# Kernel optimization log

Hardware: AMD Instinct MI355X
Metric: run time of the kernel (lower is better)

The kernel has to match this reference:

```python
import jax, jax.numpy as jnp
import numpy as np

B, N, DIM, POS, H = 8, 2048, 256, 128, 8
QK = DIM + POS  # 384
HD = DIM // H   # 32
SCALE = HD ** -0.5


def setup_inputs() -> dict:
    key = jax.random.key(0)
    ks = jax.random.split(key, 12)
    def lin(k, fan_in, fan_out):
        bound = 1.0 / np.sqrt(fan_in)
        kw, kb = jax.random.split(k)
        W = jax.random.uniform(kw, (fan_in, fan_out), jnp.float32, -bound, bound)
        b = jax.random.uniform(kb, (fan_out,), jnp.float32, -bound, bound)
        return W, b
    Wq, bq = lin(ks[0], QK, DIM)
    Wk, bk = lin(ks[1], QK, DIM)
    Wv, bv = lin(ks[2], DIM, DIM)
    Wp, bp = lin(ks[3], DIM, DIM)
    return {
        "x": jax.random.normal(ks[4], (B, N, DIM), jnp.float32),
        "pos_embed": jax.random.normal(ks[5], (B, N, POS), jnp.float32),
        "ln_g": jnp.ones((DIM,), jnp.float32),
        "ln_b": jnp.zeros((DIM,), jnp.float32),
        "Wq": Wq, "bq": bq,
        "Wk": Wk, "bk": bk,
        "Wv": Wv, "bv": bv,
        "Wp": Wp, "bp": bp,
    }


def _layernorm(x, g, b, eps=1e-5):
    mu = jnp.mean(x, axis=-1, keepdims=True)
    var = jnp.mean(jnp.square(x - mu), axis=-1, keepdims=True)
    return (x - mu) * jax.lax.rsqrt(var + eps) * g + b


def reference(x, pos_embed, ln_g, ln_b, Wq, bq, Wk, bk, Wv, bv, Wp, bp):
    short_cut = x
    xn = _layernorm(x, ln_g, ln_b)                       # [B,N,C]
    qk_in = jnp.concatenate([xn, pos_embed], axis=-1)    # [B,N,C+C']
    q = qk_in @ Wq + bq                                  # [B,N,C]
    k = qk_in @ Wk + bk
    v = xn @ Wv + bv
    def heads(t):
        return t.reshape(B, N, H, HD).transpose(0, 2, 1, 3)  # [B,H,N,d]
    q, k, v = heads(q), heads(k), heads(v)
    # scores cast to fp32 before scale+softmax, as in the original
    scores = jnp.einsum('bhid,bhjd->bhij', q, k).astype(jnp.float32) * SCALE
    attn = jax.nn.softmax(scores, axis=-1).astype(q.dtype)  # [B,H,N,N]
    out = jnp.einsum('bhij,bhjd->bhid', attn, v)             # [B,H,N,d]
    out = out.transpose(0, 2, 1, 3).reshape(B, N, DIM)       # [B,N,C]
    return short_cut + (out @ Wp + bp)
```

## Files before the change

kernel.cpp:

```cpp
#include <hip/hip_runtime.h>
#include <stdint.h>

#define DEVFN __device__ __forceinline__

typedef float f32x4 __attribute__((ext_vector_type(4)));
typedef float f32x2 __attribute__((ext_vector_type(2)));
typedef float f32x16 __attribute__((ext_vector_type(16)));
typedef short s16x8 __attribute__((ext_vector_type(8)));
typedef short s16x4 __attribute__((ext_vector_type(4)));
typedef unsigned int u32x4 __attribute__((ext_vector_type(4)));

using u32_g = __attribute__((address_space(1))) unsigned int;
using u32_l = __attribute__((address_space(3))) unsigned int;

DEVFN unsigned short f2bf(float f) {
  unsigned int u = __builtin_bit_cast(unsigned int, f);
  u += 0x7FFFu + ((u >> 16) & 1u);
  return (unsigned short)(u >> 16);
}

DEVFN f32x4 mfma16(s16x8 a, s16x8 b, f32x4 c) {
  return __builtin_amdgcn_mfma_f32_16x16x32_bf16(a, b, c, 0, 0, 0);
}

DEVFN f32x16 mfma32(s16x8 a, s16x8 b, f32x16 c) {
  return __builtin_amdgcn_mfma_f32_32x32x16_bf16(a, b, c, 0, 0, 0);
}

DEVFN void gl_lds16(const unsigned short* g, unsigned short* l) {
  __builtin_amdgcn_global_load_lds((const u32_g*)(uintptr_t)g,
                                   (u32_l*)(uintptr_t)l, 16, 0, 0);
}

#define QSCALE 0.25504370446096164f

__global__ void prep_kernel(const float* __restrict__ Wq, const float* __restrict__ bq,
                            const float* __restrict__ Wk, const float* __restrict__ bk,
                            const float* __restrict__ Wv, const float* __restrict__ bv,
                            const float* __restrict__ Wp,
                            unsigned short* __restrict__ Wt, float* __restrict__ b_all,
                            unsigned short* __restrict__ Wpt) {
  const int n = blockIdx.x;
  const int k = threadIdx.x;
  if (n < 768) {
    float v;
    if (n < 256)      v = Wq[k * 256 + n] * QSCALE;
    else if (n < 512) v = Wk[k * 256 + (n - 256)];
    else              v = (k < 256) ? Wv[k * 256 + (n - 512)] : 0.f;
    Wt[n * 384 + k] = f2bf(v);
    if (k == 0)
      b_all[n] = (n < 256) ? bq[n] * QSCALE : (n < 512) ? bk[n - 256] : bv[n - 512];
  } else {
    const int nn = n - 768;
    if (k < 256) Wpt[nn * 256 + k] = f2bf(Wp[k * 256 + nn]);
  }
}

__global__ __launch_bounds__(256) void ln_kernel(
    const float* __restrict__ x, const float* __restrict__ pos,
    const float* __restrict__ g, const float* __restrict__ b,
    unsigned short* __restrict__ qkin) {
  const int lane = threadIdx.x & 63;
  const int w = threadIdx.x >> 6;
  const long t = (long)blockIdx.x * 4 + w;
  const f32x4 xv = *(const f32x4*)(x + t * 256 + lane * 4);
  float s = xv[0] + xv[1] + xv[2] + xv[3];
#pragma unroll
  for (int m = 1; m < 64; m <<= 1) s += __shfl_xor(s, m);
  const float mu = s * (1.f / 256.f);
  f32x4 d;
  float ss = 0.f;
#pragma unroll
  for (int i = 0; i < 4; ++i) { d[i] = xv[i] - mu; ss += d[i] * d[i]; }
#pragma unroll
  for (int m = 1; m < 64; m <<= 1) ss += __shfl_xor(ss, m);
  const float rs = rsqrtf(ss * (1.f / 256.f) + 1e-5f);
  const f32x4 gv = *(const f32x4*)(g + lane * 4);
  const f32x4 bv = *(const f32x4*)(b + lane * 4);
  s16x4 ov;
#pragma unroll
  for (int i = 0; i < 4; ++i) ov[i] = (short)f2bf(d[i] * rs * gv[i] + bv[i]);
  *(s16x4*)(qkin + t * 384 + lane * 4) = ov;
  const f32x2 pv = *(const f32x2*)(pos + t * 128 + lane * 2);
  const unsigned int packed = (unsigned int)f2bf(pv[0]) | ((unsigned int)f2bf(pv[1]) << 16);
  *(unsigned int*)(qkin + t * 384 + 256 + lane * 2) = packed;
}

template <int KSTEPS64, int NBLK, bool PROJ>
__global__ __launch_bounds__(256, 2) void gemm_bt(
    const unsigned short* __restrict__ A, const unsigned short* __restrict__ Bt,
    const float* __restrict__ bias, const float* __restrict__ resid,
    unsigned short* __restrict__ Obf, unsigned short* __restrict__ VTout,
    float* __restrict__ Of) {
  constexpr int K = KSTEPS64 * 64;
  constexpr int N = NBLK * 128;
  __shared__ __align__(16) unsigned short Al[2][128 * 32];
  __shared__ __align__(16) unsigned short Bl[2][128 * 32];
  const int bid = blockIdx.x;
  const int m0 = (bid / NBLK) * 128;
  const int n0 = (bid % NBLK) * 128;
  const int tid = threadIdx.x;
  const int lane = tid & 63;
  const int ln = lane & 15, hi = lane >> 4;
  const int wid = tid >> 6;
  const int wm = (wid >> 1) * 64, wn = (wid & 1) * 64;
  f32x4 acc[4][4] = {};
  const int r0 = tid >> 2, kq = (tid & 3) * 8;
  for (int kt = 0; kt < KSTEPS64; ++kt) {
    const int k0 = kt * 64;
    __syncthreads();
#pragma unroll
    for (int s = 0; s < 2; ++s) {
      gl_lds16(A + (long)(m0 + r0) * K + k0 + s * 32 + kq, Al[s] + tid * 8);
      gl_lds16(A + (long)(m0 + 64 + r0) * K + k0 + s * 32 + kq, Al[s] + (tid + 256) * 8);
      gl_lds16(Bt + (long)(n0 + r0) * K + k0 + s * 32 + kq, Bl[s] + tid * 8);
      gl_lds16(Bt + (long)(n0 + 64 + r0) * K + k0 + s * 32 + kq, Bl[s] + (tid + 256) * 8);
    }
    __syncthreads();
#pragma unroll
    for (int s = 0; s < 2; ++s) {
      s16x8 af[4], bfr[4];
#pragma unroll
      for (int m = 0; m < 4; ++m) af[m] = *(const s16x8*)(Al[s] + (wm + m * 16 + ln) * 32 + hi * 8);
#pragma unroll
      for (int n = 0; n < 4; ++n) bfr[n] = *(const s16x8*)(Bl[s] + (wn + n * 16 + ln) * 32 + hi * 8);
#pragma unroll
      for (int m = 0; m < 4; ++m)
#pragma unroll
        for (int n = 0; n < 4; ++n) acc[m][n] = mfma16(af[m], bfr[n], acc[m][n]);
    }
  }
#pragma unroll
  for (int m = 0; m < 4; ++m)
#pragma unroll
    for (int n = 0; n < 4; ++n) {
      const int col = n0 + wn + n * 16 + ln;
      const float bv = bias[col];
      if constexpr (PROJ) {
#pragma unroll
        for (int r = 0; r < 4; ++r) {
          const long row = m0 + wm + m * 16 + hi * 4 + r;
          Of[row * N + col] = acc[m][n][r] + bv + resid[row * N + col];
        }
      } else if (n0 < 512) {
#pragma unroll
        for (int r = 0; r < 4; ++r) {
          const long row = m0 + wm + m * 16 + hi * 4 + r;
          Obf[row * 512 + col] = f2bf(acc[m][n][r] + bv);
        }
      } else {
        const int hd = col - 512;
        const int hh = hd >> 5, dd = hd & 31;
        const int t0 = m0 + wm + m * 16 + hi * 4;
        const int bb = t0 >> 11, tl = t0 & 2047;
        const int tperm = (tl & ~12) | ((tl & 4) << 1) | ((tl & 8) >> 1);
        s16x4 pk;
#pragma unroll
        for (int r = 0; r < 4; ++r) pk[r] = (short)f2bf(acc[m][n][r] + bv);
        *(s16x4*)(VTout + ((size_t)(bb * 8 + hh) * 32 + dd) * 2048 + tperm) = pk;
      }
    }
}

__global__ __launch_bounds__(256, 4) void attn_fa4(
    const unsigned short* __restrict__ QK, const unsigned short* __restrict__ VT,
    unsigned short* __restrict__ AO) {
  __shared__ __align__(16) unsigned short Kl[2][64 * 32];
  __shared__ __align__(16) unsigned short Vl[2][32 * 64];
  const int phys = blockIdx.x;
  const int lb = (phys & 7) * 128 + (phys >> 3);
  const int bh = lb >> 4, qt = lb & 15;
  const int b = bh >> 3, h = bh & 7;
  const long tokbase = (long)b * 2048;
  const unsigned short* QKb = QK + tokbase * 512;
  const unsigned short* VTb = VT + (size_t)bh * 32 * 2048;
  const int tid = threadIdx.x, lane = tid & 63, w = tid >> 6;
  const int qi = lane & 31, hb = lane >> 5;
  const int q0 = qt * 128 + w * 32;

  s16x8 qf0, qf1;
  {
    const unsigned short* qp = QKb + (long)(q0 + qi) * 512 + h * 32 + hb * 8;
    qf0 = *(const s16x8*)(qp);
    qf1 = *(const s16x8*)(qp + 16);
  }

  const int kc = w * 64 + lane;
  const int kr = kc >> 2, ksl = kc & 3;
  const unsigned short* ksrc0 = QKb + (long)kr * 512 + 256 + h * 32 + ((ksl ^ ((kr >> 1) & 3)) * 8);
  const int vd = kc >> 3, vsl = kc & 7;
  const unsigned short* vsrc0 = VTb + vd * 2048 + ((vsl ^ (vd & 7)) * 8);

  f32x16 O = {};
  f32x16 L = {};
  float mrun = 0.f;
  const int ksw = (qi >> 1) & 3;
  const int vsw = qi & 7;

  s16x8 onesB;
#pragma unroll
  for (int i = 0; i < 8; ++i) onesB[i] = (short)0x3F80;

  gl_lds16(ksrc0, &Kl[0][0] + kc * 8);
  gl_lds16(vsrc0, &Vl[0][0] + kc * 8);
  __syncthreads();

  int buf = 0;
  for (int t = 0; t < 32; ++t) {
    if (t < 31) {
      const long kv0 = (long)(t + 1) * 64;
      gl_lds16(ksrc0 + kv0 * 512, &Kl[buf ^ 1][0] + kc * 8);
      gl_lds16(vsrc0 + kv0, &Vl[buf ^ 1][0] + kc * 8);
    }
    const char* KB = (const char*)&Kl[buf][0];
    const char* VB = (const char*)&Vl[buf][0];
    const s16x8 k00 = *(const s16x8*)(KB + qi * 64 + ((hb ^ ksw) << 4));
    const s16x8 k01 = *(const s16x8*)(KB + qi * 64 + (((2 + hb) ^ ksw) << 4));
    const s16x8 k10 = *(const s16x8*)(KB + (32 + qi) * 64 + ((hb ^ ksw) << 4));
    const s16x8 k11 = *(const s16x8*)(KB + (32 + qi) * 64 + (((2 + hb) ^ ksw) << 4));
    f32x16 s0 = {}, s1 = {};
    s0 = mfma32(k00, qf0, s0);
    s0 = mfma32(k01, qf1, s0);
    s1 = mfma32(k10, qf0, s1);
    s1 = mfma32(k11, qf1, s1);
    float tm[16];
#pragma unroll
    for (int r = 0; r < 16; ++r) tm[r] = fmaxf(s0[r], s1[r]);
#pragma unroll
    for (int st = 8; st > 0; st >>= 1)
#pragma unroll
      for (int r = 0; r < st; ++r) tm[r] = fmaxf(tm[r], tm[r + st]);
    float pm = fmaxf(tm[0], __shfl_xor(tm[0], 32));
    if (!__all(pm <= mrun + 8.f)) {
      const float mnew = fmaxf(mrun, pm);
      const float f = __builtin_amdgcn_exp2f(mrun - mnew);
#pragma unroll
      for (int r = 0; r < 16; ++r) {
        const int qr = (r & 3) + 8 * (r >> 2) + 4 * hb;
        const float fr = __shfl(f, qr + (lane & 32), 64);
        O[r] *= fr;
        L[r] *= fr;
      }
      mrun = mnew;
    }
#pragma unroll
    for (int r = 0; r < 16; ++r) {
      s0[r] = __builtin_amdgcn_exp2f(s0[r] - mrun);
      s1[r] = __builtin_amdgcn_exp2f(s1[r] - mrun);
    }
    unsigned int g[16];
#pragma unroll
    for (int gi = 0; gi < 8; ++gi) {
      g[gi] = __builtin_amdgcn_perm(__builtin_bit_cast(unsigned int, s0[2 * gi + 1]),
                                    __builtin_bit_cast(unsigned int, s0[2 * gi]),
                                    0x07060302u);
      g[8 + gi] = __builtin_amdgcn_perm(__builtin_bit_cast(unsigned int, s1[2 * gi + 1]),
                                        __builtin_bit_cast(unsigned int, s1[2 * gi]),
                                        0x07060302u);
    }
    const s16x8 pa0 = __builtin_bit_cast(s16x8, (u32x4){g[0], g[1], g[2], g[3]});
    const s16x8 pa1 = __builtin_bit_cast(s16x8, (u32x4){g[4], g[5], g[6], g[7]});
    const s16x8 pa2 = __builtin_bit_cast(s16x8, (u32x4){g[8], g[9], g[10], g[11]});
    const s16x8 pa3 = __builtin_bit_cast(s16x8, (u32x4){g[12], g[13], g[14], g[15]});
    const int vrow = qi << 7;
    const s16x8 vf0 = *(const s16x8*)(VB + vrow + (((0 + hb) ^ vsw) << 4));
    const s16x8 vf1 = *(const s16x8*)(VB + vrow + (((2 + hb) ^ vsw) << 4));
    const s16x8 vf2 = *(const s16x8*)(VB + vrow + (((4 + hb) ^ vsw) << 4));
    const s16x8 vf3 = *(const s16x8*)(VB + vrow + (((6 + hb) ^ vsw) << 4));
    __builtin_amdgcn_s_setprio(1);
    O = mfma32(pa0, vf0, O);
    L = mfma32(pa0, onesB, L);
    O = mfma32(pa1, vf1, O);
    L = mfma32(pa1, onesB, L);
    O = mfma32(pa2, vf2, O);
    L = mfma32(pa2, onesB, L);
    O = mfma32(pa3, vf3, O);
    L = mfma32(pa3, onesB, L);
    __builtin_amdgcn_s_setprio(0);
    if (t < 31) {
      __syncthreads();
      buf ^= 1;
    }
  }
#pragma unroll
  for (int r = 0; r < 16; ++r) {
    const int qr = (r & 3) + 8 * (r >> 2) + 4 * hb;
    AO[(tokbase + q0 + qr) * 256 + h * 32 + qi] = f2bf(O[r] / L[r]);
  }
}

extern "C" void kernel_launch(void* const* d_in, const int* in_sizes, int n_in,
                              void* d_out, int out_size, void* d_ws, size_t ws_size,
                              hipStream_t stream) {
  (void)in_sizes; (void)n_in; (void)out_size; (void)ws_size;
  const float* x    = (const float*)d_in[0];
  const float* pos  = (const float*)d_in[1];
  const float* ln_g = (const float*)d_in[2];
  const float* ln_b = (const float*)d_in[3];
  const float* Wq   = (const float*)d_in[4];
  const float* bq   = (const float*)d_in[5];
  const float* Wk   = (const float*)d_in[6];
  const float* bk   = (const float*)d_in[7];
  const float* Wv   = (const float*)d_in[8];
  const float* bv   = (const float*)d_in[9];
  const float* Wp   = (const float*)d_in[10];
  const float* bp   = (const float*)d_in[11];
  float* out = (float*)d_out;

  unsigned short* ws   = (unsigned short*)d_ws;
  unsigned short* qkin = ws;
  unsigned short* Wt   = qkin + (long)16384 * 384;
  unsigned short* Wpt  = Wt + 768 * 384;
  unsigned short* QKb  = Wpt + 256 * 256;
  unsigned short* VT   = QKb + (long)16384 * 512;
  unsigned short* AO   = VT + (long)64 * 32 * 2048;
  float* b_all = (float*)(AO + (long)16384 * 256);

  prep_kernel<<<1024, 384, 0, stream>>>(Wq, bq, Wk, bk, Wv, bv, Wp, Wt, b_all, Wpt);
  ln_kernel<<<4096, 256, 0, stream>>>(x, pos, ln_g, ln_b, qkin);
  gemm_bt<6, 6, false><<<768, 256, 0, stream>>>(qkin, Wt, b_all, nullptr, QKb, VT, nullptr);
  attn_fa4<<<1024, 256, 0, stream>>>(QKb, VT, AO);
  gemm_bt<4, 2, true><<<256, 256, 0, stream>>>(AO, Wpt, bp, x, nullptr, nullptr, out);
}
```

Measured before the change: 99.24 us.

## Double attention KV tile to 128 per barrier and swizzle GEMM block order

The attention kernel now stages 128 keys and values per double-buffered iteration instead of 64, processing two 64-key sub-tiles between barriers. This halves the number of __syncthreads and global-to-LDS load rounds, and widens the V LDS row and XOR swizzle to match. The GEMM kernels remap block IDs with an XCD-style interleave so neighbouring tiles land on the same chiplet for better L2 reuse. LDS per block doubles, which could limit occupancy at 4 blocks per CU.

```diff
diff --git a/kernel.cpp b/kernel.cpp
--- a/kernel.cpp
+++ b/kernel.cpp
@@ -94,9 +94,11 @@
     float* __restrict__ Of) {
   constexpr int K = KSTEPS64 * 64;
   constexpr int N = NBLK * 128;
+  constexpr int NWG = 128 * NBLK;
   __shared__ __align__(16) unsigned short Al[2][128 * 32];
   __shared__ __align__(16) unsigned short Bl[2][128 * 32];
-  const int bid = blockIdx.x;
+  const int bid0 = blockIdx.x;
+  const int bid = (bid0 & 7) * (NWG >> 3) + (bid0 >> 3);
   const int m0 = (bid / NBLK) * 128;
   const int n0 = (bid % NBLK) * 128;
   const int tid = threadIdx.x;
@@ -162,11 +164,11 @@
     }
 }
 
-__global__ __launch_bounds__(256, 4) void attn_fa4(
+__global__ __launch_bounds__(256, 4) void attn_fa5(
     const unsigned short* __restrict__ QK, const unsigned short* __restrict__ VT,
     unsigned short* __restrict__ AO) {
-  __shared__ __align__(16) unsigned short Kl[2][64 * 32];
-  __shared__ __align__(16) unsigned short Vl[2][32 * 64];
+  __shared__ __align__(16) unsigned short Kl[2][128 * 32];
+  __shared__ __align__(16) unsigned short Vl[2][32 * 128];
   const int phys = blockIdx.x;
   const int lb = (phys & 7) * 128 + (phys >> 3);
   const int bh = lb >> 4, qt = lb & 15;
@@ -185,99 +187,107 @@
     qf1 = *(const s16x8*)(qp + 16);
   }
 
-  const int kc = w * 64 + lane;
-  const int kr = kc >> 2, ksl = kc & 3;
+  const int kr = tid >> 2, ksl = tid & 3;
   const unsigned short* ksrc0 = QKb + (long)kr * 512 + 256 + h * 32 + ((ksl ^ ((kr >> 1) & 3)) * 8);
-  const int vd = kc >> 3, vsl = kc & 7;
-  const unsigned short* vsrc0 = VTb + vd * 2048 + ((vsl ^ (vd & 7)) * 8);
+  const int vd = tid >> 4, vsl = tid & 15;
+  const unsigned short* vsrc0 = VTb + (long)vd * 2048 + ((vsl ^ (vd & 15)) * 8);
 
   f32x16 O = {};
   f32x16 L = {};
   float mrun = 0.f;
   const int ksw = (qi >> 1) & 3;
-  const int vsw = qi & 7;
+  const int vsw = qi & 15;
 
   s16x8 onesB;
 #pragma unroll
   for (int i = 0; i < 8; ++i) onesB[i] = (short)0x3F80;
 
-  gl_lds16(ksrc0, &Kl[0][0] + kc * 8);
-  gl_lds16(vsrc0, &Vl[0][0] + kc * 8);
+  gl_lds16(ksrc0, &Kl[0][0] + tid * 8);
+  gl_lds16(ksrc0 + (long)64 * 512, &Kl[0][0] + (tid + 256) * 8);
+  gl_lds16(vsrc0, &Vl[0][0] + tid * 8);
+  gl_lds16(vsrc0 + (long)16 * 2048, &Vl[0][0] + (tid + 256) * 8);
   __syncthreads();
 
   int buf = 0;
-  for (int t = 0; t < 32; ++t) {
-    if (t < 31) {
-      const long kv0 = (long)(t + 1) * 64;
-      gl_lds16(ksrc0 + kv0 * 512, &Kl[buf ^ 1][0] + kc * 8);
-      gl_lds16(vsrc0 + kv0, &Vl[buf ^ 1][0] + kc * 8);
+  for (int t = 0; t < 16; ++t) {
+    if (t < 15) {
+      const long kv0 = (long)(t + 1) * 128;
+      gl_lds16(ksrc0 + kv0 * 512, &Kl[buf ^ 1][0] + tid * 8);
+      gl_lds16(ksrc0 + (kv0 + 64) * 512, &Kl[buf ^ 1][0] + (tid + 256) * 8);
+      gl_lds16(vsrc0 + kv0, &Vl[buf ^ 1][0] + tid * 8);
+      gl_lds16(vsrc0 + (long)16 * 2048 + kv0, &Vl[buf ^ 1][0] + (tid + 256) * 8);
     }
     const char* KB = (const char*)&Kl[buf][0];
     const char* VB = (const char*)&Vl[buf][0];
-    const s16x8 k00 = *(const s16x8*)(KB + qi * 64 + ((hb ^ ksw) << 4));
-    const s16x8 k01 = *(const s16x8*)(KB + qi * 64 + (((2 + hb) ^ ksw) << 4));
-    const s16x8 k10 = *(const s16x8*)(KB + (32 + qi) * 64 + ((hb ^ ksw) << 4));
-    const s16x8 k11 = *(const s16x8*)(KB + (32 + qi) * 64 + (((2 + hb) ^ ksw) << 4));
-    f32x16 s0 = {}, s1 = {};
-    s0 = mfma32(k00, qf0, s0);
-    s0 = mfma32(k01, qf1, s0);
-    s1 = mfma32(k10, qf0, s1);
-    s1 = mfma32(k11, qf1, s1);
-    float tm[16];
-#pragma unroll
-    for (int r = 0; r < 16; ++r) tm[r] = fmaxf(s0[r], s1[r]);
-#pragma unroll
-    for (int st = 8; st > 0; st >>= 1)
-#pragma unroll
-      for (int r = 0; r < st; ++r) tm[r] = fmaxf(tm[r], tm[r + st]);
-    float pm = fmaxf(tm[0], __shfl_xor(tm[0], 32));
-    if (!__all(pm <= mrun + 8.f)) {
-      const float mnew = fmaxf(mrun, pm);
-      const float f = __builtin_amdgcn_exp2f(mrun - mnew);
+#pragma unroll
+    for (int h2 = 0; h2 < 2; ++h2) {
+      const int tb = h2 * 64;
+      const s16x8 ka0 = *(const s16x8*)(KB + (tb + qi) * 64 + ((hb ^ ksw) << 4));
+      const s16x8 ka1 = *(const s16x8*)(KB + (tb + qi) * 64 + (((2 + hb) ^ ksw) << 4));
+      const s16x8 kb0 = *(const s16x8*)(KB + (tb + 32 + qi) * 64 + ((hb ^ ksw) << 4));
+      const s16x8 kb1 = *(const s16x8*)(KB + (tb + 32 + qi) * 64 + (((2 + hb) ^ ksw) << 4));
+      f32x16 s0 = {}, s1 = {};
+      s0 = mfma32(ka0, qf0, s0);
+      s0 = mfma32(ka1, qf1, s0);
+      s1 = mfma32(kb0, qf0, s1);
+      s1 = mfma32(kb1, qf1, s1);
+      float u[8];
+#pragma unroll
+      for (int r = 0; r < 8; ++r) u[r] = fmaxf(s0[r], s0[r + 8]);
+#pragma unroll
+      for (int r = 0; r < 8; ++r) u[r] = fmaxf(u[r], fmaxf(s1[r], s1[r + 8]));
+      const float pa = fmaxf(fmaxf(u[0], u[1]), u[2]);
+      const float pb = fmaxf(fmaxf(u[3], u[4]), u[5]);
+      float pm = fmaxf(fmaxf(pa, u[6]), fmaxf(pb, u[7]));
+      pm = fmaxf(pm, __shfl_xor(pm, 32));
+      if (!__all(pm <= mrun + 8.f)) {
+        const float mnew = fmaxf(mrun, pm);
+        const float f = __builtin_amdgcn_exp2f(mrun - mnew);
+#pragma unroll
+        for (int r = 0; r < 16; ++r) {
+          const int qr = (r & 3) + 8 * (r >> 2) + 4 * hb;
+          const float fr = __shfl(f, qr + (lane & 32), 64);
+          O[r] *= fr;
+          L[r] *= fr;
+        }
+        mrun = mnew;
+      }
 #pragma unroll
       for (int r = 0; r < 16; ++r) {
-        const int qr = (r & 3) + 8 * (r >> 2) + 4 * hb;
-        const float fr = __shfl(f, qr + (lane & 32), 64);
-        O[r] *= fr;
-        L[r] *= fr;
+        s0[r] = __builtin_amdgcn_exp2f(s0[r] - mrun);
+        s1[r] = __builtin_amdgcn_exp2f(s1[r] - mrun);
       }
-      mrun = mnew;
-    }
-#pragma unroll
-    for (int r = 0; r < 16; ++r) {
-      s0[r] = __builtin_amdgcn_exp2f(s0[r] - mrun);
-      s1[r] = __builtin_amdgcn_exp2f(s1[r] - mrun);
-    }
-    unsigned int g[16];
-#pragma unroll
-    for (int gi = 0; gi < 8; ++gi) {
-      g[gi] = __builtin_amdgcn_perm(__builtin_bit_cast(unsigned int, s0[2 * gi + 1]),
-                                    __builtin_bit_cast(unsigned int, s0[2 * gi]),
-                                    0x07060302u);
-      g[8 + gi] = __builtin_amdgcn_perm(__builtin_bit_cast(unsigned int, s1[2 * gi + 1]),
-                                        __builtin_bit_cast(unsigned int, s1[2 * gi]),
-                                        0x07060302u);
-    }
-    const s16x8 pa0 = __builtin_bit_cast(s16x8, (u32x4){g[0], g[1], g[2], g[3]});
-    const s16x8 pa1 = __builtin_bit_cast(s16x8, (u32x4){g[4], g[5], g[6], g[7]});
-    const s16x8 pa2 = __builtin_bit_cast(s16x8, (u32x4){g[8], g[9], g[10], g[11]});
-    const s16x8 pa3 = __builtin_bit_cast(s16x8, (u32x4){g[12], g[13], g[14], g[15]});
-    const int vrow = qi << 7;
-    const s16x8 vf0 = *(const s16x8*)(VB + vrow + (((0 + hb) ^ vsw) << 4));
-    const s16x8 vf1 = *(const s16x8*)(VB + vrow + (((2 + hb) ^ vsw) << 4));
-    const s16x8 vf2 = *(const s16x8*)(VB + vrow + (((4 + hb) ^ vsw) << 4));
-    const s16x8 vf3 = *(const s16x8*)(VB + vrow + (((6 + hb) ^ vsw) << 4));
-    __builtin_amdgcn_s_setprio(1);
-    O = mfma32(pa0, vf0, O);
-    L = mfma32(pa0, onesB, L);
-    O = mfma32(pa1, vf1, O);
-    L = mfma32(pa1, onesB, L);
-    O = mfma32(pa2, vf2, O);
-    L = mfma32(pa2, onesB, L);
-    O = mfma32(pa3, vf3, O);
-    L = mfma32(pa3, onesB, L);
-    __builtin_amdgcn_s_setprio(0);
-    if (t < 31) {
+      unsigned int g[16];
+#pragma unroll
+      for (int gi = 0; gi < 8; ++gi) {
+        g[gi] = __builtin_amdgcn_perm(__builtin_bit_cast(unsigned int, s0[2 * gi + 1]),
+                                      __builtin_bit_cast(unsigned int, s0[2 * gi]),
+                                      0x07060302u);
+        g[8 + gi] = __builtin_amdgcn_perm(__builtin_bit_cast(unsigned int, s1[2 * gi + 1]),
+                                          __builtin_bit_cast(unsigned int, s1[2 * gi]),
+                                          0x07060302u);
+      }
+      const s16x8 pa0 = __builtin_bit_cast(s16x8, (u32x4){g[0], g[1], g[2], g[3]});
+      const s16x8 pa1 = __builtin_bit_cast(s16x8, (u32x4){g[4], g[5], g[6], g[7]});
+      const s16x8 pa2 = __builtin_bit_cast(s16x8, (u32x4){g[8], g[9], g[10], g[11]});
+      const s16x8 pa3 = __builtin_bit_cast(s16x8, (u32x4){g[12], g[13], g[14], g[15]});
+      const int vrow = qi << 8;
+      const s16x8 vf0 = *(const s16x8*)(VB + vrow + (((h2 * 8 + 0 + hb) ^ vsw) << 4));
+      const s16x8 vf1 = *(const s16x8*)(VB + vrow + (((h2 * 8 + 2 + hb) ^ vsw) << 4));
+      const s16x8 vf2 = *(const s16x8*)(VB + vrow + (((h2 * 8 + 4 + hb) ^ vsw) << 4));
+      const s16x8 vf3 = *(const s16x8*)(VB + vrow + (((h2 * 8 + 6 + hb) ^ vsw) << 4));
+      __builtin_amdgcn_s_setprio(1);
+      O = mfma32(pa0, vf0, O);
+      L = mfma32(pa0, onesB, L);
+      O = mfma32(pa1, vf1, O);
+      L = mfma32(pa1, onesB, L);
+      O = mfma32(pa2, vf2, O);
+      L = mfma32(pa2, onesB, L);
+      O = mfma32(pa3, vf3, O);
+      L = mfma32(pa3, onesB, L);
+      __builtin_amdgcn_s_setprio(0);
+    }
+    if (t < 15) {
       __syncthreads();
       buf ^= 1;
     }
@@ -319,6 +329,6 @@
   prep_kernel<<<1024, 384, 0, stream>>>(Wq, bq, Wk, bk, Wv, bv, Wp, Wt, b_all, Wpt);
   ln_kernel<<<4096, 256, 0, stream>>>(x, pos, ln_g, ln_b, qkin);
   gemm_bt<6, 6, false><<<768, 256, 0, stream>>>(qkin, Wt, b_all, nullptr, QKb, VT, nullptr);
-  attn_fa4<<<1024, 256, 0, stream>>>(QKb, VT, AO);
+  attn_fa5<<<1024, 256, 0, stream>>>(QKb, VT, AO);
   gemm_bt<4, 2, true><<<256, 256, 0, stream>>>(AO, Wpt, bp, x, nullptr, nullptr, out);
 }
```

Result: faster. 96.38 us (-2.9%).
